# Kernel tuning notes

Hardware: AMD Instinct MI355X
Metric: run time of the kernel (lower is better)

## Reference

```python
import jax, jax.numpy as jnp
import numpy as np

V, EMB, H, N, E, B = 100000, 300, 64, 20000, 160000, 4096
L, T = 2, 3  # layer_timesteps = [3, 3]


def setup_inputs() -> dict:
    key = jax.random.key(0)
    ks = jax.random.split(key, 24)
    ri = lambda k, shape, hi: jax.random.randint(k, shape, 0, hi)
    rn = lambda k, shape, s=0.05: (jax.random.normal(k, shape, dtype=jnp.float32) * s)
    emb_table = rn(ks[7], (V, EMB), 0.1).at[0].set(0.0)  # padding_idx=0 row is zeros
    return {
        'emb_ind0': ri(ks[0], (N,), V),
        'emb_ind1': ri(ks[1], (N,), V),
        'adj0': ri(ks[2], (E, 2), N),
        'adj1': ri(ks[3], (E, 2), N),
        'prop_ind0': ri(ks[4], (B,), N),
        'prop_ind1': ri(ks[5], (B,), N),
        'labels': ri(ks[6], (B,), 2),
        'emb_table': emb_table,
        'proj_W': rn(ks[8], (EMB, H)),   # emb_proj weight (stored input-major)
        'proj_b': jnp.zeros((H,), jnp.float32),
        'msg_W': rn(ks[9], (L, H, H)),   # per-layer edge-type-0 message linear
        'msg_b': jnp.zeros((L, H), jnp.float32),
        'gru_Wih': rn(ks[10], (L, 3 * H, H)),
        'gru_Whh': rn(ks[11], (L, 3 * H, H)),
        'gru_bih': jnp.zeros((L, 3 * H), jnp.float32),
        'gru_bhh': jnp.zeros((L, 3 * H), jnp.float32),
        'cla_W1': rn(ks[12], (2 * H, 16)),
        'cla_b1': jnp.zeros((16,), jnp.float32),
        'cla_W2': rn(ks[13], (16, 1)),
        'cla_b2': jnp.zeros((1,), jnp.float32),
    }


def _gru_cell(x, h, Wih, Whh, bih, bhh):
    # torch.nn.GRUCell math
    gi = x @ Wih.T + bih
    gh = h @ Whh.T + bhh
    i_r, i_z, i_n = jnp.split(gi, 3, axis=-1)
    h_r, h_z, h_n = jnp.split(gh, 3, axis=-1)
    r = jax.nn.sigmoid(i_r + h_r)
    z = jax.nn.sigmoid(i_z + h_z)
    n = jnp.tanh(i_n + r * h_n)
    return (1.0 - z) * n + z * h


def reference(emb_ind0, emb_ind1, adj0, adj1, prop_ind0, prop_ind1, labels,
              emb_table, proj_W, proj_b, msg_W, msg_b,
              gru_Wih, gru_Whh, gru_bih, gru_bhh,
              cla_W1, cla_b1, cla_W2, cla_b2):
    def ggnn(x, adj):
        src, tgt = adj[:, 0], adj[:, 1]
        h = x
        for l in range(L):              # 2 structurally distinct layers
            for _ in range(T):          # 3 timesteps each
                m = h[src] @ msg_W[l] + msg_b[l]                     # [E, H] gather + transform
                inc = jax.ops.segment_sum(m, tgt, num_segments=N)    # scatter-add messages
                h = _gru_cell(inc, h, gru_Wih[l], gru_Whh[l], gru_bih[l], gru_bhh[l])
        return h

    def branch(emb_ind, adj, prop_ind):
        ge = emb_table[emb_ind]          # embedding lookup [N, EMB]
        ge = ge @ proj_W + proj_b        # emb_proj -> [N, H]
        ge = ggnn(ge, adj)
        return ge[prop_ind]              # index_select -> [B, H]

    g0 = branch(emb_ind0, adj0, prop_ind0)
    g1 = branch(emb_ind1, adj1, prop_ind1)
    ge = jnp.concatenate([g0, g1], axis=-1)                 # match='concat' -> [B, 2H]
    hid = jax.nn.relu(ge @ cla_W1 + cla_b1)
    logits = jax.nn.sigmoid(hid @ cla_W2 + cla_b2)          # [B, 1], num_class=1 path
    p = logits.squeeze(-1)
    y = labels.astype(p.dtype)
    eps = 1e-7  # mirrors torch BCELoss log-clamping
    loss = -jnp.mean(y * jnp.log(jnp.clip(p, eps, 1.0))
                     + (1.0 - y) * jnp.log(jnp.clip(1.0 - p, eps, 1.0)))
    return logits, loss
```

## Files before the change

### kernel.cpp

```cpp
#include <hip/hip_runtime.h>
#include <hip/hip_bf16.h>

typedef unsigned short u16;
typedef __attribute__((ext_vector_type(8))) short s16x8;
typedef __attribute__((ext_vector_type(4))) float f32x4;

#define NN 20000
#define HH 64
#define EMBD 300
#define EE 160000
#define BB 4096
#define NODES 40000

#define OFF_PROJB 0
#define OFF_MSGB  64
#define OFF_BIH   192
#define OFF_BHH   576
#define OFF_CW1T  960
#define OFF_CB1   3008
#define OFF_CW2   3024
#define OFF_CB2   3040
#define PARAM_SZ  3072

#define PB_WIH   0
#define PB_WHH   24576
#define PB_WMT   49152
#define PB_PROJT 57344
#define PB_SZ    77824

#define APAD 344

__device__ __forceinline__ float b2f(u16 u) {
    union { unsigned int i; float f; } v; v.i = ((unsigned int)u) << 16; return v.f;
}
__device__ __forceinline__ u16 f2b(float f) {
    union { float f; unsigned int u; } v; v.f = f;
    unsigned int u = v.u;
    return (u16)((u + 0x7FFFu + ((u >> 16) & 1u)) >> 16);
}
__device__ __forceinline__ float ldf(const void* p, long long i, int isbf) {
    return isbf ? b2f(((const u16*)p)[i]) : ((const float*)p)[i];
}
__device__ __forceinline__ u16 ldb(const void* p, long long i, int isbf) {
    return isbf ? ((const u16*)p)[i] : f2b(((const float*)p)[i]);
}
__device__ __forceinline__ void stf(void* p, long long i, int isbf, float v) {
    if (isbf) ((u16*)p)[i] = f2b(v);
    else      ((float*)p)[i] = v;
}

__global__ void sniff_kernel(const u16* probe, int* flag)
{
    if (threadIdx.x == 0 && blockIdx.x == 0) {
        int good = 0;
        for (int i = 0; i < 128; i += 2) {
            unsigned int e = (probe[i] >> 7) & 0xFF;
            if (e >= 105 && e <= 127) good++;
        }
        *flag = (good >= 48) ? 1 : 0;
    }
}

__global__ __launch_bounds__(256) void conv_kernel(
    const void* projW, const void* projb, const void* msgW, const void* msgb,
    const void* wih, const void* whh, const void* bih, const void* bhh,
    const void* cw1, const void* cb1, const void* cw2, const void* cb2,
    float* P, u16* PB, const int* flag)
{
    int isbf = *flag;
    int i = blockIdx.x * 256 + threadIdx.x;
    if (i < 64)    P[OFF_PROJB + i] = ldf(projb, i, isbf);
    if (i < 128)   P[OFF_MSGB + i]  = ldf(msgb, i, isbf);
    if (i < 384)   { P[OFF_BIH + i] = ldf(bih, i, isbf); P[OFF_BHH + i] = ldf(bhh, i, isbf); }
    if (i < 2048)  { int t = i >> 7, k = i & 127; P[OFF_CW1T + i] = ldf(cw1, (long long)k * 16 + t, isbf); }
    if (i < 16)    { P[OFF_CB1 + i] = ldf(cb1, i, isbf); P[OFF_CW2 + i] = ldf(cw2, i, isbf); }
    if (i == 0)    P[OFF_CB2] = ldf(cb2, 0, isbf);

    if (i < 24576) {
        int l = i / 12288, r = i - l * 12288;
        int frag = r >> 9, rr = r & 511, lane = rr >> 3, e = rr & 7;
        int jt = frag >> 1, kt = frag & 1;
        int srow = jt * 16 + (lane & 15);
        int sk = kt * 32 + ((lane >> 4) << 3) + e;
        long long si = (long long)l * 12288 + srow * 64 + sk;
        PB[PB_WIH + i] = ldb(wih, si, isbf);
        PB[PB_WHH + i] = ldb(whh, si, isbf);
    }
    if (i < 8192) {
        int l = i >> 12, r = i & 4095;
        int frag = r >> 9, rr = r & 511, lane = rr >> 3, e = rr & 7;
        int jt = frag >> 1, kt = frag & 1;
        int srow = jt * 16 + (lane & 15);
        int sk = kt * 32 + ((lane >> 4) << 3) + e;
        PB[PB_WMT + i] = ldb(msgW, (long long)l * 4096 + sk * 64 + srow, isbf);
    }
    if (i < 20480) {
        int frag = i >> 9, rr = i & 511, lane = rr >> 3, e = rr & 7;
        int jt = frag / 10, kt = frag - jt * 10;
        int srow = jt * 16 + (lane & 15);
        int sk = kt * 32 + ((lane >> 4) << 3) + e;
        PB[PB_PROJT + i] = (sk < 300) ? ldb(projW, (long long)sk * 64 + srow, isbf) : (u16)0;
    }
}

__global__ __launch_bounds__(256) void hist_kernel(const int* __restrict__ adj0,
                                                   const int* __restrict__ adj1, int* off)
{
    int e = blockIdx.x * 256 + threadIdx.x;
    if (e >= 2 * EE) return;
    int b = e / EE, le = e - b * EE;
    const int* adj = b ? adj1 : adj0;
    int tgt = adj[2 * le + 1];
    atomicAdd(&off[b * (NN + 1) + tgt + 1], 1);
}

__global__ __launch_bounds__(1024) void scan_kernel(int* off, int* cursor)
{
    int b = blockIdx.x;
    int* o = off + (size_t)b * (NN + 1);
    int* cur = cursor + (size_t)b * NN;
    __shared__ int wsum[16];
    __shared__ int wscan[16];
    int tid = threadIdx.x, wv = tid >> 6, lane = tid & 63;
    int base = 0;
    for (int start = 0; start < NN; start += 1024) {
        int i = start + tid;
        int v = (i < NN) ? o[i + 1] : 0;
        int orig = v;
        #pragma unroll
        for (int d = 1; d < 64; d <<= 1) {
            int t = __shfl_up(v, d);
            if (lane >= d) v += t;
        }
        if (lane == 63) wsum[wv] = v;
        __syncthreads();
        if (tid < 16) {
            int w = wsum[tid];
            #pragma unroll
            for (int d = 1; d < 16; d <<= 1) {
                int t = __shfl_up(w, d, 16);
                if (tid >= d) w += t;
            }
            wscan[tid] = w;
        }
        __syncthreads();
        int woff = (wv == 0) ? 0 : wscan[wv - 1];
        int excl = base + woff + v - orig;
        if (i < NN) { o[i] = excl; cur[i] = excl; }
        base += wscan[15];
    }
    if (tid == 0) o[NN] = base;
}

__global__ __launch_bounds__(256) void scatter_kernel(const int* __restrict__ adj0,
                                                      const int* __restrict__ adj1,
                                                      int* cursor, int* esrc)
{
    int e = blockIdx.x * 256 + threadIdx.x;
    if (e >= 2 * EE) return;
    int b = e / EE, le = e - b * EE;
    const int* adj = b ? adj1 : adj0;
    int src = adj[2 * le + 0];
    int tgt = adj[2 * le + 1];
    int pos = atomicAdd(&cursor[b * NN + tgt], 1);
    esrc[(size_t)b * EE + pos] = src;
}

__global__ __launch_bounds__(256) void projm_kernel(const void* emb,
                                                    const int* __restrict__ i0,
                                                    const int* __restrict__ i1,
                                                    const float* __restrict__ P,
                                                    const u16* __restrict__ PB,
                                                    u16* __restrict__ h, const int* flag)
{
    __shared__ u16 sA[64 * APAD];
    int isbf = *flag;
    int tid = threadIdx.x;
    int node0 = blockIdx.x * 64;

    {
        int r = tid >> 2, sub = tid & 3;
        int n = node0 + r;
        int b = n >= NN;
        int ln = n - b * NN;
        int idx = b ? i1[ln] : i0[ln];
        if (isbf) {
            const ushort4* src = (const ushort4*)((const u16*)emb + (size_t)idx * EMBD);
            ushort4* dst = (ushort4*)(sA + r * APAD);
            for (int c = sub; c < 75; c += 4) dst[c] = src[c];
            if (sub == 0) {
                ushort4 z = {0, 0, 0, 0};
                for (int c = 75; c < 80; ++c) dst[c] = z;
            }
        } else {
            const float* src = (const float*)emb + (size_t)idx * EMBD;
            for (int k = sub; k < 300; k += 4) sA[r * APAD + k] = f2b(src[k]);
            if (sub == 0) for (int k = 300; k < 320; ++k) sA[r * APAD + k] = 0;
        }
    }

    int wv = tid >> 6, lane = tid & 63, quad = lane >> 4, cn = lane & 15;
    int m0 = wv * 16;
    f32x4 acc[4];
    #pragma unroll
    for (int j = 0; j < 4; ++j) {
        float bb = P[OFF_PROJB + j * 16 + cn];
        acc[j] = {bb, bb, bb, bb};
    }
    #pragma unroll
    for (int kt = 0; kt < 10; ++kt) {
        s16x8 a = *(const s16x8*)&sA[(m0 + cn) * APAD + kt * 32 + quad * 8];
        #pragma unroll
        for (int j = 0; j < 4; ++j) {
            s16x8 bfr = *(const s16x8*)&PB[PB_PROJT + (j * 10 + kt) * 512 + lane * 8];
            acc[j] = __builtin_amdgcn_mfma_f32_16x16x32_bf16(a, bfr, acc[j], 0, 0, 0);
        }
    }
    #pragma unroll
    for (int j = 0; j < 4; ++j)
        #pragma unroll
        for (int r = 0; r < 4; ++r)
            h[(size_t)(node0 + m0 + quad * 4 + r) * 64 + j * 16 + cn] = f2b(acc[j][r]);
}

__global__ __launch_bounds__(256) void fstep_kernel(const u16* __restrict__ h_old,
                                                    u16* __restrict__ h_new,
                                                    const int* __restrict__ ioff,
                                                    const int* __restrict__ esrc,
                                                    const float* __restrict__ P,
                                                    const u16* __restrict__ PB, int l)
{
    __shared__ u16 s_S[32 * 64];
    __shared__ u16 s_h[32 * 64];
    __shared__ float s_deg[32];

    int tid = threadIdx.x;
    int node0 = blockIdx.x * 32;

    {
        int team = tid >> 3, oct = tid & 7;
        int node = node0 + team;
        int br = node >= NN;
        int ln = node - br * NN;
        const int* o = ioff + (size_t)br * (NN + 1);
        int s0 = o[ln], s1 = o[ln + 1];
        const int* es = esrc + (size_t)br * EE;
        const u16* hb = h_old + (size_t)br * NN * 64;

        *(uint4*)&s_h[team * 64 + oct * 8] =
            *(const uint4*)&h_old[(size_t)node * 64 + oct * 8];
        if (oct == 0) s_deg[team] = (float)(s1 - s0);

        float acc[8];
        #pragma unroll
        for (int k = 0; k < 8; ++k) acc[k] = 0.f;

        int base = s0, rem = s1 - s0;
        while (rem > 0) {
            int cnt = rem < 8 ? rem : 8;
            int myidx = es[base + (oct < cnt ? oct : cnt - 1)];
            #pragma unroll
            for (int j = 0; j < 8; ++j) {
                int e = __shfl(myidx, j, 8);
                uint4 v = *(const uint4*)&hb[(size_t)e * 64 + oct * 8];
                float w = (j < cnt) ? 1.f : 0.f;
                #pragma unroll
                for (int p = 0; p < 4; ++p) {
                    unsigned int u = ((const unsigned int*)&v)[p];
                    union { unsigned int i; float f; } lo, hi;
                    lo.i = u << 16; hi.i = u & 0xffff0000u;
                    acc[2 * p]     += w * lo.f;
                    acc[2 * p + 1] += w * hi.f;
                }
            }
            base += cnt;
            rem -= cnt;
        }

        u16 pk[8];
        #pragma unroll
        for (int k = 0; k < 8; ++k) pk[k] = f2b(acc[k]);
        *(uint4*)&s_S[team * 64 + oct * 8] = *(const uint4*)pk;
    }
    __syncthreads();

    int wv = tid >> 6, lane = tid & 63;
    int wr = wv >> 1, wc = wv & 1;
    int m0 = wr * 16;
    int quad = lane >> 4, cn = lane & 15;
    int arow = (m0 + cn) * 64 + quad * 8;
    int fl = lane * 8;

    s16x8 aS0 = *(const s16x8*)&s_S[arow];
    s16x8 aS1 = *(const s16x8*)&s_S[arow + 32];
    s16x8 aH0 = *(const s16x8*)&s_h[arow];
    s16x8 aH1 = *(const s16x8*)&s_h[arow + 32];
    __syncthreads();

    const u16* WM = PB + PB_WMT + (size_t)l * 4096;
    #pragma unroll
    for (int jtl = 0; jtl < 2; ++jtl) {
        int jt = wc * 2 + jtl;
        float mb = P[OFF_MSGB + l * 64 + jt * 16 + cn];
        f32x4 acc;
        acc[0] = s_deg[m0 + quad * 4 + 0] * mb;
        acc[1] = s_deg[m0 + quad * 4 + 1] * mb;
        acc[2] = s_deg[m0 + quad * 4 + 2] * mb;
        acc[3] = s_deg[m0 + quad * 4 + 3] * mb;
        acc = __builtin_amdgcn_mfma_f32_16x16x32_bf16(aS0, *(const s16x8*)&WM[(jt * 2 + 0) * 512 + fl], acc, 0, 0, 0);
        acc = __builtin_amdgcn_mfma_f32_16x16x32_bf16(aS1, *(const s16x8*)&WM[(jt * 2 + 1) * 512 + fl], acc, 0, 0, 0);
        #pragma unroll
        for (int r = 0; r < 4; ++r)
            s_S[(m0 + quad * 4 + r) * 64 + jt * 16 + cn] = f2b(acc[r]);
    }
    __syncthreads();

    s16x8 aI0 = *(const s16x8*)&s_S[arow];
    s16x8 aI1 = *(const s16x8*)&s_S[arow + 32];
    __syncthreads();

    const u16* WI = PB + PB_WIH + (size_t)l * 12288;
    const u16* WH = PB + PB_WHH + (size_t)l * 12288;
    const float* bi = P + OFF_BIH + l * 192;
    const float* bh = P + OFF_BHH + l * 192;

    #pragma unroll
    for (int cl = 0; cl < 2; ++cl) {
        int jt = wc * 2 + cl;
        int j0 = jt * 16;
        float vr = bi[j0 + cn], vz = bi[64 + j0 + cn], vn = bi[128 + j0 + cn];
        float wr_ = bh[j0 + cn], wz = bh[64 + j0 + cn], wn = bh[128 + j0 + cn];
        f32x4 gr = {vr, vr, vr, vr}, gz = {vz, vz, vz, vz}, gn = {vn, vn, vn, vn};
        f32x4 hr = {wr_, wr_, wr_, wr_}, hz = {wz, wz, wz, wz}, hn = {wn, wn, wn, wn};
        int fr = (jt * 2) * 512 + fl, frz = ((4 + jt) * 2) * 512 + fl, frn = ((8 + jt) * 2) * 512 + fl;
        gr = __builtin_amdgcn_mfma_f32_16x16x32_bf16(aI0, *(const s16x8*)&WI[fr], gr, 0, 0, 0);
        gr = __builtin_amdgcn_mfma_f32_16x16x32_bf16(aI1, *(const s16x8*)&WI[fr + 512], gr, 0, 0, 0);
        gz = __builtin_amdgcn_mfma_f32_16x16x32_bf16(aI0, *(const s16x8*)&WI[frz], gz, 0, 0, 0);
        gz = __builtin_amdgcn_mfma_f32_16x16x32_bf16(aI1, *(const s16x8*)&WI[frz + 512], gz, 0, 0, 0);
        gn = __builtin_amdgcn_mfma_f32_16x16x32_bf16(aI0, *(const s16x8*)&WI[frn], gn, 0, 0, 0);
        gn = __builtin_amdgcn_mfma_f32_16x16x32_bf16(aI1, *(const s16x8*)&WI[frn + 512], gn, 0, 0, 0);
        hr = __builtin_amdgcn_mfma_f32_16x16x32_bf16(aH0, *(const s16x8*)&WH[fr], hr, 0, 0, 0);
        hr = __builtin_amdgcn_mfma_f32_16x16x32_bf16(aH1, *(const s16x8*)&WH[fr + 512], hr, 0, 0, 0);
        hz = __builtin_amdgcn_mfma_f32_16x16x32_bf16(aH0, *(const s16x8*)&WH[frz], hz, 0, 0, 0);
        hz = __builtin_amdgcn_mfma_f32_16x16x32_bf16(aH1, *(const s16x8*)&WH[frz + 512], hz, 0, 0, 0);
        hn = __builtin_amdgcn_mfma_f32_16x16x32_bf16(aH0, *(const s16x8*)&WH[frn], hn, 0, 0, 0);
        hn = __builtin_amdgcn_mfma_f32_16x16x32_bf16(aH1, *(const s16x8*)&WH[frn + 512], hn, 0, 0, 0);
        #pragma unroll
        for (int r = 0; r < 4; ++r) {
            int row = m0 + quad * 4 + r;
            float rr = 1.f / (1.f + __expf(-(gr[r] + hr[r])));
            float zz = 1.f / (1.f + __expf(-(gz[r] + hz[r])));
            float nn = tanhf(gn[r] + rr * hn[r]);
            float ho = b2f(s_h[row * 64 + j0 + cn]);
            s_S[row * 64 + j0 + cn] = f2b((1.f - zz) * nn + zz * ho);
        }
    }
    __syncthreads();

    {
        int team = tid >> 3, oct = tid & 7;
        int node = node0 + team;
        *(uint4*)&h_new[(size_t)node * 64 + oct * 8] =
            *(const uint4*)&s_S[team * 64 + oct * 8];
    }
}

__global__ __launch_bounds__(256) void cls_kernel(const u16* __restrict__ h,
                                                  const int* __restrict__ p0,
                                                  const int* __restrict__ p1,
                                                  const int* __restrict__ labels,
                                                  const float* __restrict__ P,
                                                  void* out, float* partial, const int* flag)
{
    int isbf = *flag;
    int wv = threadIdx.x >> 6, lane = threadIdx.x & 63;
    int s = blockIdx.x * 4 + wv;
    int n0 = p0[s], n1 = p1[s];
    float f0 = b2f(h[(size_t)n0 * 64 + lane]);
    float f1 = b2f(h[(size_t)(NN + n1) * 64 + lane]);
    float z = P[OFF_CB2];
    #pragma unroll
    for (int t = 0; t < 16; ++t) {
        float part = f0 * P[OFF_CW1T + t * 128 + lane] + f1 * P[OFF_CW1T + t * 128 + 64 + lane];
        #pragma unroll
        for (int off = 32; off; off >>= 1) part += __shfl_xor(part, off);
        z += fmaxf(part + P[OFF_CB1 + t], 0.f) * P[OFF_CW2 + t];
    }
    float p = 1.f / (1.f + expf(-z));
    float y = (float)labels[s];
    const float eps = 1e-7f;
    float pc  = fminf(fmaxf(p, eps), 1.f);
    float pc1 = fminf(fmaxf(1.f - p, eps), 1.f);
    float term = y * logf(pc) + (1.f - y) * logf(pc1);
    __shared__ float red[4];
    if (lane == 0) { stf(out, s, isbf, p); red[wv] = term; }
    __syncthreads();
    if (threadIdx.x == 0) partial[blockIdx.x] = red[0] + red[1] + red[2] + red[3];
}

__global__ __launch_bounds__(256) void loss_kernel(const float* __restrict__ partial,
                                                   void* out, const int* flag)
{
    __shared__ float red[256];
    int tid = threadIdx.x;
    float s = 0.f;
    for (int i = tid; i < 1024; i += 256) s += partial[i];
    red[tid] = s;
    __syncthreads();
    for (int d = 128; d > 0; d >>= 1) {
        if (tid < d) red[tid] += red[tid + d];
        __syncthreads();
    }
    if (tid == 0) stf(out, BB, *flag, -red[0] / (float)BB);
}

extern "C" void kernel_launch(void* const* d_in, const int* in_sizes, int n_in,
                              void* d_out, int out_size, void* d_ws, size_t ws_size,
                              hipStream_t stream)
{
    const int* adj0   = (const int*)d_in[2];
    const int* adj1   = (const int*)d_in[3];
    const int* prop0  = (const int*)d_in[4];
    const int* prop1  = (const int*)d_in[5];
    const int* labels = (const int*)d_in[6];

    int* flag = (int*)d_ws;
    float* P  = (float*)d_ws + 16;
    u16* PB   = (u16*)(P + PARAM_SZ);
    u16* h0   = (u16*)(((uintptr_t)(PB + PB_SZ) + 255) & ~(uintptr_t)255);
    u16* h1   = h0 + (size_t)NODES * 64;
    float* partial = (float*)(h1 + (size_t)NODES * 64);
    int* ioff   = (int*)(partial + 1024);
    int* cursor = ioff + 2 * (NN + 1) + 62;
    int* esrc   = cursor + 2 * NN;

    hipMemsetAsync(ioff, 0, 2 * (NN + 1) * sizeof(int), stream);

    sniff_kernel<<<1, 64, 0, stream>>>((const u16*)d_in[8], flag);
    conv_kernel<<<96, 256, 0, stream>>>(d_in[8], d_in[9], d_in[10], d_in[11], d_in[12], d_in[13],
                                        d_in[14], d_in[15], d_in[16], d_in[17], d_in[18], d_in[19],
                                        P, PB, flag);
    hist_kernel<<<(2 * EE) / 256, 256, 0, stream>>>(adj0, adj1, ioff);
    scan_kernel<<<2, 1024, 0, stream>>>(ioff, cursor);
    scatter_kernel<<<(2 * EE) / 256, 256, 0, stream>>>(adj0, adj1, cursor, esrc);
    projm_kernel<<<(2 * NN) / 64, 256, 0, stream>>>(d_in[7], (const int*)d_in[0],
                                                    (const int*)d_in[1], P, PB, h0, flag);

    u16* hcur = h0;
    u16* hnext = h1;
    for (int l = 0; l < 2; ++l) {
        for (int t = 0; t < 3; ++t) {
            fstep_kernel<<<NODES / 32, 256, 0, stream>>>(hcur, hnext, ioff, esrc, P, PB, l);
            u16* tmp = hcur; hcur = hnext; hnext = tmp;
        }
    }

    cls_kernel<<<BB / 4, 256, 0, stream>>>(hcur, prop0, prop1, labels, P, d_out, partial, flag);
    loss_kernel<<<1, 256, 0, stream>>>(partial, d_out, flag);
}
```

Measured before the change: 392.8 us.

## Fold sniff, memset and loss kernels into neighbors; swizzle fstep block mapping

```diff
diff --git a/kernel.cpp b/kernel.cpp
--- a/kernel.cpp
+++ b/kernel.cpp
@@ -30,6 +30,8 @@
 
 #define APAD 344
 
+#define ZCNT (16 + 2 * (NN + 1))
+
 __device__ __forceinline__ float b2f(u16 u) {
     union { unsigned int i; float f; } v; v.i = ((unsigned int)u) << 16; return v.f;
 }
@@ -49,26 +51,26 @@
     else      ((float*)p)[i] = v;
 }
 
-__global__ void sniff_kernel(const u16* probe, int* flag)
-{
-    if (threadIdx.x == 0 && blockIdx.x == 0) {
-        int good = 0;
-        for (int i = 0; i < 128; i += 2) {
-            unsigned int e = (probe[i] >> 7) & 0xFF;
-            if (e >= 105 && e <= 127) good++;
-        }
-        *flag = (good >= 48) ? 1 : 0;
-    }
+__device__ __forceinline__ int sniff_inline(const u16* probe, int tid)
+{
+    u16 x = probe[2 * (tid & 63)];
+    unsigned int e = (x >> 7) & 0xFF;
+    unsigned long long m = __ballot(e >= 105 && e <= 127);
+    return (__popcll(m) >= 48) ? 1 : 0;
 }
 
 __global__ __launch_bounds__(256) void conv_kernel(
     const void* projW, const void* projb, const void* msgW, const void* msgb,
     const void* wih, const void* whh, const void* bih, const void* bhh,
     const void* cw1, const void* cb1, const void* cw2, const void* cb2,
-    float* P, u16* PB, const int* flag)
-{
-    int isbf = *flag;
-    int i = blockIdx.x * 256 + threadIdx.x;
+    float* P, u16* PB, int* zbase)
+{
+    int tid = threadIdx.x;
+    int isbf = sniff_inline((const u16*)projW, tid);
+    int i = blockIdx.x * 256 + tid;
+
+    if (i < ZCNT) zbase[i] = 0;
+
     if (i < 64)    P[OFF_PROJB + i] = ldf(projb, i, isbf);
     if (i < 128)   P[OFF_MSGB + i]  = ldf(msgb, i, isbf);
     if (i < 384)   { P[OFF_BIH + i] = ldf(bih, i, isbf); P[OFF_BHH + i] = ldf(bhh, i, isbf); }
@@ -122,10 +124,19 @@
     __shared__ int wsum[16];
     __shared__ int wscan[16];
     int tid = threadIdx.x, wv = tid >> 6, lane = tid & 63;
+
+    int vpre[20];
+    #pragma unroll
+    for (int c = 0; c < 20; ++c) {
+        int i = c * 1024 + tid;
+        vpre[c] = (i < NN) ? o[i + 1] : 0;
+    }
+
     int base = 0;
-    for (int start = 0; start < NN; start += 1024) {
-        int i = start + tid;
-        int v = (i < NN) ? o[i + 1] : 0;
+    #pragma unroll 1
+    for (int c = 0; c < 20; ++c) {
+        int i = c * 1024 + tid;
+        int v = vpre[c];
         int orig = v;
         #pragma unroll
         for (int d = 1; d < 64; d <<= 1) {
@@ -171,11 +182,12 @@
                                                     const int* __restrict__ i1,
                                                     const float* __restrict__ P,
                                                     const u16* __restrict__ PB,
-                                                    u16* __restrict__ h, const int* flag)
+                                                    u16* __restrict__ h,
+                                                    const u16* __restrict__ probe)
 {
     __shared__ u16 sA[64 * APAD];
-    int isbf = *flag;
     int tid = threadIdx.x;
+    int isbf = sniff_inline(probe, tid);
     int node0 = blockIdx.x * 64;
 
     {
@@ -193,9 +205,17 @@
                 for (int c = 75; c < 80; ++c) dst[c] = z;
             }
         } else {
-            const float* src = (const float*)emb + (size_t)idx * EMBD;
-            for (int k = sub; k < 300; k += 4) sA[r * APAD + k] = f2b(src[k]);
-            if (sub == 0) for (int k = 300; k < 320; ++k) sA[r * APAD + k] = 0;
+            const float4* src = (const float4*)((const float*)emb + (size_t)idx * EMBD);
+            ushort4* dst = (ushort4*)(sA + r * APAD);
+            for (int c = sub; c < 75; c += 4) {
+                float4 f = src[c];
+                ushort4 o4 = { f2b(f.x), f2b(f.y), f2b(f.z), f2b(f.w) };
+                dst[c] = o4;
+            }
+            if (sub == 0) {
+                ushort4 z = {0, 0, 0, 0};
+                for (int c = 75; c < 80; ++c) dst[c] = z;
+            }
         }
     }
 
@@ -235,7 +255,11 @@
     __shared__ float s_deg[32];
 
     int tid = threadIdx.x;
-    int node0 = blockIdx.x * 32;
+    int bsw = blockIdx.x;
+    int half = (bsw >> 2) & 1;
+    int t = (bsw >> 3) * 4 + (bsw & 3);
+    if (t >= 625) return;
+    int node0 = half * NN + t * 32;
 
     {
         int team = tid >> 3, oct = tid & 7;
@@ -370,10 +394,13 @@
                                                   const int* __restrict__ p1,
                                                   const int* __restrict__ labels,
                                                   const float* __restrict__ P,
-                                                  void* out, float* partial, const int* flag)
-{
-    int isbf = *flag;
-    int wv = threadIdx.x >> 6, lane = threadIdx.x & 63;
+                                                  void* out, float* partial,
+                                                  int* donecnt,
+                                                  const u16* __restrict__ probe)
+{
+    int tid = threadIdx.x;
+    int isbf = sniff_inline(probe, tid);
+    int wv = tid >> 6, lane = tid & 63;
     int s = blockIdx.x * 4 + wv;
     int n0 = p0[s], n1 = p1[s];
     float f0 = b2f(h[(size_t)n0 * 64 + lane]);
@@ -395,23 +422,25 @@
     __shared__ float red[4];
     if (lane == 0) { stf(out, s, isbf, p); red[wv] = term; }
     __syncthreads();
-    if (threadIdx.x == 0) partial[blockIdx.x] = red[0] + red[1] + red[2] + red[3];
-}
-
-__global__ __launch_bounds__(256) void loss_kernel(const float* __restrict__ partial,
-                                                   void* out, const int* flag)
-{
-    __shared__ float red[256];
-    int tid = threadIdx.x;
-    float s = 0.f;
-    for (int i = tid; i < 1024; i += 256) s += partial[i];
-    red[tid] = s;
-    __syncthreads();
-    for (int d = 128; d > 0; d >>= 1) {
-        if (tid < d) red[tid] += red[tid + d];
+    if (tid == 0) partial[blockIdx.x] = red[0] + red[1] + red[2] + red[3];
+
+    __shared__ int amlast;
+    __threadfence();
+    if (tid == 0) amlast = (atomicAdd(donecnt, 1) == (BB / 4) - 1);
+    __syncthreads();
+    if (amlast) {
+        __threadfence();
+        __shared__ float red2[256];
+        float ss = 0.f;
+        for (int i2 = tid; i2 < 1024; i2 += 256) ss += partial[i2];
+        red2[tid] = ss;
         __syncthreads();
-    }
-    if (tid == 0) stf(out, BB, *flag, -red[0] / (float)BB);
+        for (int d = 128; d > 0; d >>= 1) {
+            if (tid < d) red2[tid] += red2[tid + d];
+            __syncthreads();
+        }
+        if (tid == 0) stf(out, BB, isbf, -red2[0] / (float)BB);
+    }
 }
 
 extern "C" void kernel_launch(void* const* d_in, const int* in_sizes, int n_in,
@@ -423,38 +452,37 @@
     const int* prop0  = (const int*)d_in[4];
     const int* prop1  = (const int*)d_in[5];
     const int* labels = (const int*)d_in[6];
-
-    int* flag = (int*)d_ws;
+    const u16* probe  = (const u16*)d_in[8];
+
     float* P  = (float*)d_ws + 16;
     u16* PB   = (u16*)(P + PARAM_SZ);
     u16* h0   = (u16*)(((uintptr_t)(PB + PB_SZ) + 255) & ~(uintptr_t)255);
     u16* h1   = h0 + (size_t)NODES * 64;
     float* partial = (float*)(h1 + (size_t)NODES * 64);
-    int* ioff   = (int*)(partial + 1024);
+    int* zbase  = (int*)(partial + 1024);
+    int* donecnt = zbase;
+    int* ioff   = zbase + 16;
     int* cursor = ioff + 2 * (NN + 1) + 62;
     int* esrc   = cursor + 2 * NN;
 
-    hipMemsetAsync(ioff, 0, 2 * (NN + 1) * sizeof(int), stream);
-
-    sniff_kernel<<<1, 64, 0, stream>>>((const u16*)d_in[8], flag);
-    conv_kernel<<<96, 256, 0, stream>>>(d_in[8], d_in[9], d_in[10], d_in[11], d_in[12], d_in[13],
-                                        d_in[14], d_in[15], d_in[16], d_in[17], d_in[18], d_in[19],
-                                        P, PB, flag);
+    conv_kernel<<<157, 256, 0, stream>>>(d_in[8], d_in[9], d_in[10], d_in[11], d_in[12], d_in[13],
+                                         d_in[14], d_in[15], d_in[16], d_in[17], d_in[18], d_in[19],
+                                         P, PB, zbase);
     hist_kernel<<<(2 * EE) / 256, 256, 0, stream>>>(adj0, adj1, ioff);
     scan_kernel<<<2, 1024, 0, stream>>>(ioff, cursor);
     scatter_kernel<<<(2 * EE) / 256, 256, 0, stream>>>(adj0, adj1, cursor, esrc);
     projm_kernel<<<(2 * NN) / 64, 256, 0, stream>>>(d_in[7], (const int*)d_in[0],
-                                                    (const int*)d_in[1], P, PB, h0, flag);
+                                                    (const int*)d_in[1], P, PB, h0, probe);
 
     u16* hcur = h0;
     u16* hnext = h1;
     for (int l = 0; l < 2; ++l) {
         for (int t = 0; t < 3; ++t) {
-            fstep_kernel<<<NODES / 32, 256, 0, stream>>>(hcur, hnext, ioff, esrc, P, PB, l);
+            fstep_kernel<<<1256, 256, 0, stream>>>(hcur, hnext, ioff, esrc, P, PB, l);
             u16* tmp = hcur; hcur = hnext; hnext = tmp;
         }
     }
 
-    cls_kernel<<<BB / 4, 256, 0, stream>>>(hcur, prop0, prop1, labels, P, d_out, partial, flag);
-    loss_kernel<<<1, 256, 0, stream>>>(partial, d_out, flag);
-}
+    cls_kernel<<<BB / 4, 256, 0, stream>>>(hcur, prop0, prop1, labels, P, d_out,
+                                           partial, donecnt, probe);
+}
```

Result: slower. 448.6 us (+14.2%).
